# Optimization experiments

Measured on AMD Instinct MI355X. Metric: run time of the kernel, lower is better.

The kernel has to match this reference:

```python
import jax, jax.numpy as jnp
import numpy as np

NUM_LAYERS = 3
IN_C, HID_C, OUT_C = 128, 128, 64
N_NODES, N_EDGES = 100000, 1600000


def setup_inputs() -> dict:
    key = jax.random.key(0)
    ks = jax.random.split(key, 8)
    x = jax.random.normal(ks[0], (N_NODES, IN_C), dtype=jnp.float32)
    edge_index = jax.random.randint(ks[1], (2, N_EDGES), 0, N_NODES, dtype=jnp.int64)
    s_in = 1.0 / np.sqrt(IN_C)
    s_h = 1.0 / np.sqrt(HID_C)
    W_in = jax.random.uniform(ks[2], (IN_C, HID_C), jnp.float32, -s_in, s_in)
    W_convs = jax.random.uniform(ks[3], (NUM_LAYERS, HID_C, HID_C), jnp.float32, -s_h, s_h)
    b_convs = jax.random.uniform(ks[4], (NUM_LAYERS, HID_C), jnp.float32, -s_h, s_h)
    W_fc = jax.random.uniform(ks[5], (HID_C, OUT_C), jnp.float32, -s_h, s_h)
    b_fc = jax.random.uniform(ks[6], (OUT_C,), jnp.float32, -s_h, s_h)
    return {"x": x, "edge_index": edge_index, "W_in": W_in, "W_convs": W_convs,
            "b_convs": b_convs, "W_fc": W_fc, "b_fc": b_fc}


def _g2_tau(x_new, row, col, num_nodes):
    # per-edge squared L2 difference of gated features (p=2)
    d = x_new[row] - x_new[col]            # [E, H]
    diffs = jnp.sum(d * d, axis=-1)        # [E]
    tau_vals = jax.ops.segment_sum(diffs, row, num_segments=num_nodes)
    deg = jax.ops.segment_sum(jnp.ones_like(diffs), row, num_segments=num_nodes) + 1e-10
    return jnp.tanh(tau_vals / deg)[:, None]  # [N, 1]


def reference(x, edge_index, W_in, W_convs, b_convs, W_fc, b_fc):
    row, col = edge_index[0], edge_index[1]
    n = x.shape[0]
    x = x @ W_in                                            # input_fc (no bias)
    for l in range(NUM_LAYERS):
        h = x @ W_convs[l]                                  # GCNConv linear
        agg = jax.ops.segment_sum(h[row], col, num_segments=n) + b_convs[l]
        x_new = jax.nn.relu(agg)
        tau = _g2_tau(x_new, row, col, n)
        x = (1.0 - tau) * x + tau * x_new
    return x @ W_fc + b_fc
```

## Files before the change

### kernel.cpp

```cpp
#include <hip/hip_runtime.h>
#include <hip/hip_bf16.h>

#define N_NODES 100000
#define N_EDGES 1600000
#define HID 128
#define OUTC 64
#define NLAYERS 3

#define M_PAD 100032
#define SCAN_N (2 * N_NODES)
#define SCAN_B 1024
#define SCAN_NB ((SCAN_N + SCAN_B - 1) / SCAN_B)

typedef __attribute__((ext_vector_type(8))) short short8;
typedef __attribute__((ext_vector_type(4))) float f32x4;
typedef __attribute__((ext_vector_type(2))) float f32x2;

__device__ __forceinline__ unsigned short f2b(float f) {
  return __builtin_bit_cast(unsigned short, __float2bfloat16(f));
}
__device__ __forceinline__ float blo(unsigned int u) {
  return __builtin_bit_cast(float, u << 16);
}
__device__ __forceinline__ float bhi(unsigned int u) {
  return __builtin_bit_cast(float, u & 0xffff0000u);
}

__global__ __launch_bounds__(128) void cast_w_kernel(
    const float* __restrict__ W_in, const float* __restrict__ W_convs,
    const float* __restrict__ W_fc, unsigned short* __restrict__ wt) {
  const int b = blockIdx.x;
  const int k = threadIdx.x;
  const float* src;
  unsigned short* dst;
  int n, N;
  if (b < 128) {
    n = b; N = 128; src = W_in; dst = wt + n * 128;
  } else if (b < 512) {
    const int l = (b - 128) >> 7;
    n = (b - 128) & 127; N = 128;
    src = W_convs + (size_t)l * 16384;
    dst = wt + 16384 * (1 + l) + n * 128;
  } else {
    n = b - 512; N = 64; src = W_fc; dst = wt + 65536 + n * 128;
  }
  dst[k] = f2b(src[k * N + n]);
}

template <int MODE>
__global__ __launch_bounds__(256) void gemm_mfma_kernel(
    const float* __restrict__ Xf, const unsigned short* __restrict__ Xb,
    const unsigned short* __restrict__ Wt, const float* __restrict__ bias,
    float* __restrict__ Y, unsigned short* __restrict__ Yb) {
  constexpr int NT = (MODE == 2) ? 4 : 8;
  const int wave = threadIdx.x >> 6;
  const int lane = threadIdx.x & 63;
  const int row0 = blockIdx.x * 64 + wave * 16;
  const int lm = lane & 15;
  const int lk = (lane >> 4) * 8;

  f32x4 acc[NT];
#pragma unroll
  for (int t = 0; t < NT; ++t) acc[t] = {0.f, 0.f, 0.f, 0.f};

  const int arow = row0 + lm;
#pragma unroll
  for (int ki = 0; ki < 4; ++ki) {
    short8 a;
    if (MODE == 0) {
      float av[8];
      const bool ok = arow < N_NODES;
#pragma unroll
      for (int j = 0; j < 8; ++j)
        av[j] = ok ? Xf[(size_t)arow * 128 + ki * 32 + lk + j] : 0.f;
#pragma unroll
      for (int j = 0; j < 8; ++j)
        a[j] = (short)f2b(av[j]);
    } else {
      a = *reinterpret_cast<const short8*>(Xb + (size_t)arow * 128 + ki * 32 + lk);
    }
#pragma unroll
    for (int t = 0; t < NT; ++t) {
      const short8 b =
          *reinterpret_cast<const short8*>(Wt + (t * 16 + lm) * 128 + ki * 32 + lk);
      acc[t] = __builtin_amdgcn_mfma_f32_16x16x32_bf16(a, b, acc[t], 0, 0, 0);
    }
  }

  const int orow = row0 + (lane >> 4) * 4;
#pragma unroll
  for (int t = 0; t < NT; ++t) {
#pragma unroll
    for (int r = 0; r < 4; ++r) {
      const int rr = orow + r;
      const int cc = t * 16 + lm;
      const float v = acc[t][r];
      if (MODE == 2) {
        if (rr < N_NODES) Y[(size_t)rr * OUTC + cc] = v + bias[cc];
      } else {
        Yb[(size_t)rr * 128 + cc] = f2b(v);
      }
    }
  }
}

__global__ __launch_bounds__(256) void count_kernel(
    const int* __restrict__ row, const int* __restrict__ col,
    int* __restrict__ counts, unsigned int* __restrict__ ranks) {
  const int e = blockIdx.x * 256 + threadIdx.x;
  if (e >= N_EDGES) return;
  const int pr = atomicAdd(counts + row[e], 1);
  const int pc = atomicAdd(counts + N_NODES + col[e], 1);
  ranks[e] = (unsigned)pr | ((unsigned)pc << 16);
}

__global__ __launch_bounds__(SCAN_B) void scan1_kernel(
    const int* __restrict__ counts, int* __restrict__ incl,
    int* __restrict__ bsum) {
  __shared__ int tmp[SCAN_B];
  const int i = blockIdx.x * SCAN_B + threadIdx.x;
  tmp[threadIdx.x] = (i < SCAN_N) ? counts[i] : 0;
  __syncthreads();
  for (int d = 1; d < SCAN_B; d <<= 1) {
    int t = (threadIdx.x >= d) ? tmp[threadIdx.x - d] : 0;
    __syncthreads();
    tmp[threadIdx.x] += t;
    __syncthreads();
  }
  if (i < SCAN_N) incl[i] = tmp[threadIdx.x];
  if (threadIdx.x == SCAN_B - 1) bsum[blockIdx.x] = tmp[SCAN_B - 1];
}

__global__ __launch_bounds__(256) void scan2_kernel(int* __restrict__ bsum) {
  __shared__ int tmp[256];
  tmp[threadIdx.x] = (threadIdx.x < SCAN_NB) ? bsum[threadIdx.x] : 0;
  __syncthreads();
  for (int d = 1; d < 256; d <<= 1) {
    int t = (threadIdx.x >= d) ? tmp[threadIdx.x - d] : 0;
    __syncthreads();
    tmp[threadIdx.x] += t;
    __syncthreads();
  }
  if (threadIdx.x < SCAN_NB) bsum[threadIdx.x] = tmp[threadIdx.x];
}

__global__ __launch_bounds__(SCAN_B) void scan3_kernel(
    const int* __restrict__ counts, const int* __restrict__ incl,
    const int* __restrict__ bsum, int2* __restrict__ seg) {
  const int i = blockIdx.x * SCAN_B + threadIdx.x;
  if (i >= SCAN_N) return;
  const int c = counts[i];
  const int v = incl[i] + (blockIdx.x > 0 ? bsum[blockIdx.x - 1] : 0);
  seg[i] = make_int2(v - c, c);
}

__global__ __launch_bounds__(256) void fill_kernel(
    const int* __restrict__ row, const int* __restrict__ col,
    const unsigned int* __restrict__ ranks, const int2* __restrict__ seg,
    int* __restrict__ adj) {
  const int p = blockIdx.x * 256 + threadIdx.x;
  if (p * 2 >= N_EDGES) return;
  const int2 r2 = reinterpret_cast<const int2*>(row)[p];
  const int2 c2 = reinterpret_cast<const int2*>(col)[p];
  const uint2 u2 = reinterpret_cast<const uint2*>(ranks)[p];
  adj[seg[r2.x].x + (int)(u2.x & 0xffffu)] = c2.x;
  adj[seg[N_NODES + c2.x].x + (int)(u2.x >> 16)] = r2.x;
  adj[seg[r2.y].x + (int)(u2.y & 0xffffu)] = c2.y;
  adj[seg[N_NODES + c2.y].x + (int)(u2.y >> 16)] = r2.y;
}

__global__ __launch_bounds__(256) void quant_h_kernel(
    const unsigned int* __restrict__ hb, unsigned short* __restrict__ h8,
    float* __restrict__ scl) {
  const int g = blockIdx.x * 256 + threadIdx.x;
  const int n = g >> 6;
  if (n >= N_NODES) return;
  const int lane = g & 63;
  const unsigned int p = hb[(size_t)n * 64 + lane];
  const float x0 = blo(p), x1 = bhi(p);
  float m = fmaxf(fabsf(x0), fabsf(x1));
  m = fmaxf(m, __shfl_xor(m, 1));
  m = fmaxf(m, __shfl_xor(m, 2));
  m = fmaxf(m, __shfl_xor(m, 4));
  m = fmaxf(m, __shfl_xor(m, 8));
  m = fmaxf(m, __shfl_xor(m, 16));
  m = fmaxf(m, __shfl_xor(m, 32));
  const float inv = (m > 0.f) ? 127.0f / m : 0.f;
  if (lane == 0) scl[n] = m * (1.0f / 127.0f);
  const int q0 = __float2int_rn(x0 * inv);
  const int q1 = __float2int_rn(x1 * inv);
  h8[(size_t)n * 64 + lane] =
      (unsigned short)((q0 & 0xff) | ((q1 & 0xff) << 8));
}

__global__ __launch_bounds__(256) void aggregate_kernel(
    const unsigned short* __restrict__ h8, const float* __restrict__ scl,
    const int2* __restrict__ seg, const int* __restrict__ adj,
    const float* __restrict__ b, unsigned int* __restrict__ xnewb,
    unsigned short* __restrict__ xnew8) {
  const int g = blockIdx.x * 256 + threadIdx.x;
  const int n = g >> 6;
  if (n >= N_NODES) return;
  const int lane = g & 63;
  const int2 sg = seg[N_NODES + n];
  const int start = sg.x;
  const int end = sg.x + sg.y;

  float ax[8], ay[8];
#pragma unroll
  for (int j = 0; j < 8; ++j) { ax[j] = 0.f; ay[j] = 0.f; }
  int i = start;
  for (; i + 7 < end; i += 8) {
    unsigned int u[8];
    float s[8];
#pragma unroll
    for (int j = 0; j < 8; ++j) {
      const int nb = adj[i + j];
      u[j] = h8[(size_t)nb * 64 + lane];
      s[j] = scl[nb];
    }
#pragma unroll
    for (int j = 0; j < 8; ++j) {
      const float q0 = (float)(int)(signed char)(u[j] & 0xff);
      const float q1 = (float)((int)(short)(unsigned short)u[j] >> 8);
      ax[j] += q0 * s[j];
      ay[j] += q1 * s[j];
    }
  }
  for (; i < end; ++i) {
    const int nb = adj[i];
    const unsigned int u0 = h8[(size_t)nb * 64 + lane];
    const float s0 = scl[nb];
    ax[0] += (float)(int)(signed char)(u0 & 0xff) * s0;
    ay[0] += (float)((int)(short)(unsigned short)u0 >> 8) * s0;
  }
#pragma unroll
  for (int j = 4; j < 8; ++j) { ax[j - 4] += ax[j]; ay[j - 4] += ay[j]; }
  const float2 bb = *reinterpret_cast<const float2*>(b + lane * 2);
  const float ox = fmaxf(((ax[0] + ax[1]) + (ax[2] + ax[3])) + bb.x, 0.f);
  const float oy = fmaxf(((ay[0] + ay[1]) + (ay[2] + ay[3])) + bb.y, 0.f);
  xnewb[(size_t)n * 64 + lane] = (unsigned)f2b(ox) | ((unsigned)f2b(oy) << 16);
  const unsigned int p8 = __builtin_amdgcn_cvt_pk_fp8_f32(ox, oy, 0u, false);
  xnew8[(size_t)n * 64 + lane] = (unsigned short)(p8 & 0xffffu);
}

__global__ __launch_bounds__(256) void tau_update_kernel(
    const unsigned int* __restrict__ xnewb, const unsigned short* __restrict__ xnew8,
    const int2* __restrict__ seg, const int* __restrict__ adj,
    unsigned int* __restrict__ x) {
  const int g = blockIdx.x * 256 + threadIdx.x;
  const int n = g >> 6;
  if (n >= N_NODES) return;
  const int lane = g & 63;
  const int2 sg = seg[n];
  const int start = sg.x;
  const int cnt = sg.y;
  const int end = start + cnt;

  const unsigned int mp = xnewb[(size_t)n * 64 + lane];
  const float mx = blo(mp), my = bhi(mp);

  float s0 = 0.f, s1 = 0.f, s2 = 0.f, s3 = 0.f;
  int i = start;
  for (; i + 3 < end; i += 4) {
    const unsigned int u0 = xnew8[(size_t)adj[i] * 64 + lane];
    const unsigned int u1 = xnew8[(size_t)adj[i + 1] * 64 + lane];
    const unsigned int u2 = xnew8[(size_t)adj[i + 2] * 64 + lane];
    const unsigned int u3 = xnew8[(size_t)adj[i + 3] * 64 + lane];
    const f32x2 v0 = __builtin_amdgcn_cvt_pk_f32_fp8(u0, false);
    const f32x2 v1 = __builtin_amdgcn_cvt_pk_f32_fp8(u1, false);
    const f32x2 v2 = __builtin_amdgcn_cvt_pk_f32_fp8(u2, false);
    const f32x2 v3 = __builtin_amdgcn_cvt_pk_f32_fp8(u3, false);
    const float d0x = mx - v0[0], d0y = my - v0[1];
    const float d1x = mx - v1[0], d1y = my - v1[1];
    const float d2x = mx - v2[0], d2y = my - v2[1];
    const float d3x = mx - v3[0], d3y = my - v3[1];
    s0 += d0x * d0x + d0y * d0y;
    s1 += d1x * d1x + d1y * d1y;
    s2 += d2x * d2x + d2y * d2y;
    s3 += d3x * d3x + d3y * d3y;
  }
  for (; i < end; ++i) {
    const unsigned int u0 = xnew8[(size_t)adj[i] * 64 + lane];
    const f32x2 v0 = __builtin_amdgcn_cvt_pk_f32_fp8(u0, false);
    const float d0x = mx - v0[0], d0y = my - v0[1];
    s0 += d0x * d0x + d0y * d0y;
  }
  float s = (s0 + s1) + (s2 + s3);
  s += __shfl_xor(s, 1);
  s += __shfl_xor(s, 2);
  s += __shfl_xor(s, 4);
  s += __shfl_xor(s, 8);
  s += __shfl_xor(s, 16);
  s += __shfl_xor(s, 32);
  const float tau = tanhf(s / ((float)cnt + 1e-10f));

  const unsigned int xp = x[(size_t)n * 64 + lane];
  const float nx = (1.f - tau) * blo(xp) + tau * mx;
  const float ny = (1.f - tau) * bhi(xp) + tau * my;
  x[(size_t)n * 64 + lane] = (unsigned)f2b(nx) | ((unsigned)f2b(ny) << 16);
}

extern "C" void kernel_launch(void* const* d_in, const int* in_sizes, int n_in,
                              void* d_out, int out_size, void* d_ws,
                              size_t ws_size, hipStream_t stream) {
  const float* x_in = (const float*)d_in[0];
  const int* ei = (const int*)d_in[1];
  const float* W_in = (const float*)d_in[2];
  const float* W_convs = (const float*)d_in[3];
  const float* b_convs = (const float*)d_in[4];
  const float* W_fc = (const float*)d_in[5];
  const float* b_fc = (const float*)d_in[6];
  float* out = (float*)d_out;

  const int* row = ei;
  const int* col = ei + N_EDGES;

  const size_t PF = (size_t)M_PAD * HID;
  unsigned short* xb2 = (unsigned short*)d_ws;
  unsigned short* hb = xb2 + PF;
  unsigned short* xnewb = hb + PF;
  unsigned short* xnew8 = xnewb + PF;
  unsigned short* h8 = xnew8 + (size_t)N_NODES * 64;
  float* scl = (float*)(h8 + (size_t)N_NODES * 64);
  unsigned short* wt = (unsigned short*)(scl + N_NODES);
  int* counts = (int*)(wt + 73728);
  int* incl = counts + SCAN_N;
  int* bsum = incl + SCAN_N;
  int2* seg = (int2*)(bsum + 1024);
  unsigned int* ranks = (unsigned int*)(seg + SCAN_N);
  int* adj = (int*)(ranks + N_EDGES);

  const int GEMM_BLOCKS = M_PAD / 64;
  const int EDGE_BLOCKS = (N_EDGES + 255) / 256;
  const int PAIR_BLOCKS = (N_EDGES / 2 + 255) / 256;
  const int WAVE_BLOCKS = (N_NODES * 64 + 255) / 256;

  cast_w_kernel<<<576, 128, 0, stream>>>(W_in, W_convs, W_fc, wt);

  hipMemsetAsync(counts, 0, SCAN_N * sizeof(int), stream);
  count_kernel<<<EDGE_BLOCKS, 256, 0, stream>>>(row, col, counts, ranks);
  scan1_kernel<<<SCAN_NB, SCAN_B, 0, stream>>>(counts, incl, bsum);
  scan2_kernel<<<1, 256, 0, stream>>>(bsum);
  scan3_kernel<<<SCAN_NB, SCAN_B, 0, stream>>>(counts, incl, bsum, seg);
  fill_kernel<<<PAIR_BLOCKS, 256, 0, stream>>>(row, col, ranks, seg, adj);

  gemm_mfma_kernel<0><<<GEMM_BLOCKS, 256, 0, stream>>>(
      x_in, nullptr, wt, nullptr, nullptr, xb2);

  for (int l = 0; l < NLAYERS; ++l) {
    const unsigned short* wtl = wt + 16384 * (1 + l);
    const float* bl = b_convs + (size_t)l * HID;

    gemm_mfma_kernel<1><<<GEMM_BLOCKS, 256, 0, stream>>>(
        nullptr, xb2, wtl, nullptr, nullptr, hb);
    quant_h_kernel<<<WAVE_BLOCKS, 256, 0, stream>>>(
        (const unsigned int*)hb, h8, scl);
    aggregate_kernel<<<WAVE_BLOCKS, 256, 0, stream>>>(
        h8, scl, seg, adj, bl, (unsigned int*)xnewb, xnew8);
    tau_update_kernel<<<WAVE_BLOCKS, 256, 0, stream>>>(
        (const unsigned int*)xnewb, xnew8, seg, adj, (unsigned int*)xb2);
  }

  gemm_mfma_kernel<2><<<GEMM_BLOCKS, 256, 0, stream>>>(
      nullptr, xb2, wt + 65536, b_fc, out, nullptr);
}
```

Baseline: 836.2 us.

## Fuse GEMMs into graph-build kernels and pack per-edge scales with neighbor ids

The input GEMM now runs as extra blocks of the count kernel, and the first layer GEMM as extra blocks of the fill kernel, which removes two launches and lets the independent work overlap. A new per-layer edge kernel packs each neighbor's quantization scale as a truncated bf16 into the upper bits of its 17-bit node index. The aggregate kernel then needs one adjacency load per edge instead of a separate random gather of the scale. This adds an extra edge-sized pass per layer and lowers scale precision to bf16.

```diff
diff --git a/kernel.cpp b/kernel.cpp
--- a/kernel.cpp
+++ b/kernel.cpp
@@ -11,6 +11,10 @@
 #define SCAN_N (2 * N_NODES)
 #define SCAN_B 1024
 #define SCAN_NB ((SCAN_N + SCAN_B - 1) / SCAN_B)
+
+#define GEMM_BLOCKS (M_PAD / 64)
+#define EDGE_BLOCKS ((N_EDGES + 255) / 256)
+#define PAIR_BLOCKS ((N_EDGES / 2 + 255) / 256)
 
 typedef __attribute__((ext_vector_type(8))) short short8;
 typedef __attribute__((ext_vector_type(4))) float f32x4;
@@ -48,14 +52,15 @@
 }
 
 template <int MODE>
-__global__ __launch_bounds__(256) void gemm_mfma_kernel(
-    const float* __restrict__ Xf, const unsigned short* __restrict__ Xb,
+__device__ __forceinline__ void gemm_body(
+    const int gb, const float* __restrict__ Xf,
+    const unsigned short* __restrict__ Xb,
     const unsigned short* __restrict__ Wt, const float* __restrict__ bias,
     float* __restrict__ Y, unsigned short* __restrict__ Yb) {
   constexpr int NT = (MODE == 2) ? 4 : 8;
   const int wave = threadIdx.x >> 6;
   const int lane = threadIdx.x & 63;
-  const int row0 = blockIdx.x * 64 + wave * 16;
+  const int row0 = gb * 64 + wave * 16;
   const int lm = lane & 15;
   const int lk = (lane >> 4) * 8;
 
@@ -104,14 +109,28 @@
   }
 }
 
-__global__ __launch_bounds__(256) void count_kernel(
+template <int MODE>
+__global__ __launch_bounds__(256) void gemm_mfma_kernel(
+    const float* __restrict__ Xf, const unsigned short* __restrict__ Xb,
+    const unsigned short* __restrict__ Wt, const float* __restrict__ bias,
+    float* __restrict__ Y, unsigned short* __restrict__ Yb) {
+  gemm_body<MODE>(blockIdx.x, Xf, Xb, Wt, bias, Y, Yb);
+}
+
+__global__ __launch_bounds__(256) void count_gemm0_kernel(
     const int* __restrict__ row, const int* __restrict__ col,
-    int* __restrict__ counts, unsigned int* __restrict__ ranks) {
-  const int e = blockIdx.x * 256 + threadIdx.x;
-  if (e >= N_EDGES) return;
-  const int pr = atomicAdd(counts + row[e], 1);
-  const int pc = atomicAdd(counts + N_NODES + col[e], 1);
-  ranks[e] = (unsigned)pr | ((unsigned)pc << 16);
+    int* __restrict__ counts, unsigned int* __restrict__ ranks,
+    const float* __restrict__ Xf, const unsigned short* __restrict__ Wt,
+    unsigned short* __restrict__ Yb) {
+  if (blockIdx.x < EDGE_BLOCKS) {
+    const int e = blockIdx.x * 256 + threadIdx.x;
+    if (e >= N_EDGES) return;
+    const int pr = atomicAdd(counts + row[e], 1);
+    const int pc = atomicAdd(counts + N_NODES + col[e], 1);
+    ranks[e] = (unsigned)pr | ((unsigned)pc << 16);
+  } else {
+    gemm_body<0>(blockIdx.x - EDGE_BLOCKS, Xf, nullptr, Wt, nullptr, nullptr, Yb);
+  }
 }
 
 __global__ __launch_bounds__(SCAN_B) void scan1_kernel(
@@ -154,19 +173,24 @@
   seg[i] = make_int2(v - c, c);
 }
 
-__global__ __launch_bounds__(256) void fill_kernel(
+__global__ __launch_bounds__(256) void fill_gemm1_kernel(
     const int* __restrict__ row, const int* __restrict__ col,
     const unsigned int* __restrict__ ranks, const int2* __restrict__ seg,
-    int* __restrict__ adj) {
-  const int p = blockIdx.x * 256 + threadIdx.x;
-  if (p * 2 >= N_EDGES) return;
-  const int2 r2 = reinterpret_cast<const int2*>(row)[p];
-  const int2 c2 = reinterpret_cast<const int2*>(col)[p];
-  const uint2 u2 = reinterpret_cast<const uint2*>(ranks)[p];
-  adj[seg[r2.x].x + (int)(u2.x & 0xffffu)] = c2.x;
-  adj[seg[N_NODES + c2.x].x + (int)(u2.x >> 16)] = r2.x;
-  adj[seg[r2.y].x + (int)(u2.y & 0xffffu)] = c2.y;
-  adj[seg[N_NODES + c2.y].x + (int)(u2.y >> 16)] = r2.y;
+    int* __restrict__ adj, const unsigned short* __restrict__ Xb,
+    const unsigned short* __restrict__ Wt, unsigned short* __restrict__ Yb) {
+  if (blockIdx.x < PAIR_BLOCKS) {
+    const int p = blockIdx.x * 256 + threadIdx.x;
+    if (p * 2 >= N_EDGES) return;
+    const int2 r2 = reinterpret_cast<const int2*>(row)[p];
+    const int2 c2 = reinterpret_cast<const int2*>(col)[p];
+    const uint2 u2 = reinterpret_cast<const uint2*>(ranks)[p];
+    adj[seg[r2.x].x + (int)(u2.x & 0xffffu)] = c2.x;
+    adj[seg[N_NODES + c2.x].x + (int)(u2.x >> 16)] = r2.x;
+    adj[seg[r2.y].x + (int)(u2.y & 0xffffu)] = c2.y;
+    adj[seg[N_NODES + c2.y].x + (int)(u2.y >> 16)] = r2.y;
+  } else {
+    gemm_body<1>(blockIdx.x - PAIR_BLOCKS, nullptr, Xb, Wt, nullptr, nullptr, Yb);
+  }
 }
 
 __global__ __launch_bounds__(256) void quant_h_kernel(
@@ -193,44 +217,51 @@
       (unsigned short)((q0 & 0xff) | ((q1 & 0xff) << 8));
 }
 
+__global__ __launch_bounds__(256) void edge_scl_kernel(
+    const int* __restrict__ adj_agg, const float* __restrict__ scl,
+    unsigned int* __restrict__ adjs) {
+  const int i = blockIdx.x * 256 + threadIdx.x;
+  if (i >= N_EDGES) return;
+  const int id = adj_agg[i];
+  const unsigned int sb = (unsigned int)f2b(scl[id]);
+  adjs[i] = (unsigned int)id | (sb << 17);
+}
+
 __global__ __launch_bounds__(256) void aggregate_kernel(
-    const unsigned short* __restrict__ h8, const float* __restrict__ scl,
-    const int2* __restrict__ seg, const int* __restrict__ adj,
-    const float* __restrict__ b, unsigned int* __restrict__ xnewb,
-    unsigned short* __restrict__ xnew8) {
+    const unsigned short* __restrict__ h8, const unsigned int* __restrict__ adjs,
+    const int2* __restrict__ seg, const float* __restrict__ b,
+    unsigned int* __restrict__ xnewb, unsigned short* __restrict__ xnew8) {
   const int g = blockIdx.x * 256 + threadIdx.x;
   const int n = g >> 6;
   if (n >= N_NODES) return;
   const int lane = g & 63;
   const int2 sg = seg[N_NODES + n];
-  const int start = sg.x;
-  const int end = sg.x + sg.y;
+  const int start = sg.x - N_EDGES;
+  const int end = start + sg.y;
 
   float ax[8], ay[8];
 #pragma unroll
   for (int j = 0; j < 8; ++j) { ax[j] = 0.f; ay[j] = 0.f; }
   int i = start;
   for (; i + 7 < end; i += 8) {
+    unsigned int w[8];
     unsigned int u[8];
-    float s[8];
+#pragma unroll
+    for (int j = 0; j < 8; ++j) w[j] = adjs[i + j];
+#pragma unroll
+    for (int j = 0; j < 8; ++j)
+      u[j] = h8[(size_t)(w[j] & 0x1ffffu) * 64 + lane];
 #pragma unroll
     for (int j = 0; j < 8; ++j) {
-      const int nb = adj[i + j];
-      u[j] = h8[(size_t)nb * 64 + lane];
-      s[j] = scl[nb];
-    }
-#pragma unroll
-    for (int j = 0; j < 8; ++j) {
-      const float q0 = (float)(int)(signed char)(u[j] & 0xff);
-      const float q1 = (float)((int)(short)(unsigned short)u[j] >> 8);
-      ax[j] += q0 * s[j];
-      ay[j] += q1 * s[j];
+      const float s = __builtin_bit_cast(float, (w[j] & 0xfffe0000u) >> 1);
+      ax[j] += (float)(int)(signed char)(u[j] & 0xff) * s;
+      ay[j] += (float)((int)(short)(unsigned short)u[j] >> 8) * s;
     }
   }
   for (; i < end; ++i) {
-    const int nb = adj[i];
-    const unsigned int u0 = h8[(size_t)nb * 64 + lane];
-    const float s0 = scl[nb];
+    const unsigned int w0 = adjs[i];
+    const unsigned int u0 = h8[(size_t)(w0 & 0x1ffffu) * 64 + lane];
+    const float s0 = __builtin_bit_cast(float, (w0 & 0xfffe0000u) >> 1);
     ax[0] += (float)(int)(signed char)(u0 & 0xff) * s0;
     ay[0] += (float)((int)(short)(unsigned short)u0 >> 8) * s0;
   }
@@ -330,34 +361,35 @@
   int2* seg = (int2*)(bsum + 1024);
   unsigned int* ranks = (unsigned int*)(seg + SCAN_N);
   int* adj = (int*)(ranks + N_EDGES);
-
-  const int GEMM_BLOCKS = M_PAD / 64;
-  const int EDGE_BLOCKS = (N_EDGES + 255) / 256;
-  const int PAIR_BLOCKS = (N_EDGES / 2 + 255) / 256;
+  unsigned int* adjs = (unsigned int*)(adj + 2 * N_EDGES);
+
   const int WAVE_BLOCKS = (N_NODES * 64 + 255) / 256;
 
   cast_w_kernel<<<576, 128, 0, stream>>>(W_in, W_convs, W_fc, wt);
 
   hipMemsetAsync(counts, 0, SCAN_N * sizeof(int), stream);
-  count_kernel<<<EDGE_BLOCKS, 256, 0, stream>>>(row, col, counts, ranks);
+  count_gemm0_kernel<<<EDGE_BLOCKS + GEMM_BLOCKS, 256, 0, stream>>>(
+      row, col, counts, ranks, x_in, wt, xb2);
   scan1_kernel<<<SCAN_NB, SCAN_B, 0, stream>>>(counts, incl, bsum);
   scan2_kernel<<<1, 256, 0, stream>>>(bsum);
   scan3_kernel<<<SCAN_NB, SCAN_B, 0, stream>>>(counts, incl, bsum, seg);
-  fill_kernel<<<PAIR_BLOCKS, 256, 0, stream>>>(row, col, ranks, seg, adj);
-
-  gemm_mfma_kernel<0><<<GEMM_BLOCKS, 256, 0, stream>>>(
-      x_in, nullptr, wt, nullptr, nullptr, xb2);
+
+  fill_gemm1_kernel<<<PAIR_BLOCKS + GEMM_BLOCKS, 256, 0, stream>>>(
+      row, col, ranks, seg, adj, xb2, wt + 16384, hb);
 
   for (int l = 0; l < NLAYERS; ++l) {
-    const unsigned short* wtl = wt + 16384 * (1 + l);
     const float* bl = b_convs + (size_t)l * HID;
 
-    gemm_mfma_kernel<1><<<GEMM_BLOCKS, 256, 0, stream>>>(
-        nullptr, xb2, wtl, nullptr, nullptr, hb);
+    if (l > 0) {
+      gemm_mfma_kernel<1><<<GEMM_BLOCKS, 256, 0, stream>>>(
+          nullptr, xb2, wt + 16384 * (1 + l), nullptr, nullptr, hb);
+    }
     quant_h_kernel<<<WAVE_BLOCKS, 256, 0, stream>>>(
         (const unsigned int*)hb, h8, scl);
+    edge_scl_kernel<<<EDGE_BLOCKS, 256, 0, stream>>>(
+        adj + N_EDGES, scl, adjs);
     aggregate_kernel<<<WAVE_BLOCKS, 256, 0, stream>>>(
-        h8, scl, seg, adj, bl, (unsigned int*)xnewb, xnew8);
+        h8, adjs, seg, bl, (unsigned int*)xnewb, xnew8);
     tau_update_kernel<<<WAVE_BLOCKS, 256, 0, stream>>>(
         (const unsigned int*)xnewb, xnew8, seg, adj, (unsigned int*)xb2);
   }
```

Result: no change. 847.1 us (+1.3%).
